# Kernel optimization log

Measured on AMD Instinct MI355X. Metric: run time of the kernel, lower is better.

Reference implementation:

```python
import jax, jax.numpy as jnp
import numpy as np

MARGIN = 0.2
EPS = 1e-6  # torch.pairwise_distance adds eps to the difference before the norm


def setup_inputs() -> dict:
    key = jax.random.key(0)
    k1, k2, k3 = jax.random.split(key, 3)
    B, D = 8192, 128
    emb1 = jax.random.normal(k1, (B, D), dtype=jnp.float32)
    emb2 = jax.random.normal(k2, (B, D), dtype=jnp.float32)
    target = jax.random.randint(k3, (B,), 0, 2, dtype=jnp.int64)
    return {"emb1": emb1, "emb2": emb2, "target": target}


def reference(emb1, emb2, target):
    B, D = emb1.shape
    # torch.pairwise_distance(a, b) = ||a - b + EPS||_2; expand the square:
    # |a-b+eps|^2 = |a|^2 + |b|^2 - 2 a.b + 2*eps*(sum(a)-sum(b)) + D*eps^2
    sq = (
        jnp.sum(emb1 * emb1, axis=-1)[:, None]
        + jnp.sum(emb2 * emb2, axis=-1)[None, :]
        - 2.0 * (emb1 @ emb2.T)
        + 2.0 * EPS * (jnp.sum(emb1, axis=-1)[:, None] - jnp.sum(emb2, axis=-1)[None, :])
        + D * EPS * EPS
    )
    dist = jnp.sqrt(jnp.maximum(sq, 0.0))  # [B, B]: dist[i, j] = ||emb1[i] - emb2[j] + eps||

    pos = target == 1
    neg = target == 0
    # hardest positive: max over columns j with target[j]==1; hardest negative: min over target[j]==0
    pos_max = jnp.max(jnp.where(pos[None, :], dist, -jnp.inf), axis=1)  # [B]
    neg_min = jnp.min(jnp.where(neg[None, :], dist, jnp.inf), axis=1)   # [B]
    per_anchor = jnp.maximum(pos_max - neg_min + MARGIN, 0.0)
    anchor_w = pos.astype(dist.dtype)
    # mean over anchors (rows i with target[i]==1)
    return jnp.sum(per_anchor * anchor_w) / jnp.sum(anchor_w)
```

## Files before the change

kernel.cpp:

```cpp
#include <hip/hip_runtime.h>
#include <hip/hip_bf16.h>
#include <math.h>


#define DDIM   128
#define SPLITS 8
#define MARGIN 0.2f
#define EPS    1e-6f
#define SENT   1e30f

#define CHUNK_PITCH 1056
#define WAVE_SPAN   (8 * CHUNK_PITCH)
#define TILE_BYTES  (4 * WAVE_SPAN)

typedef unsigned short ushort_t;
typedef __attribute__((ext_vector_type(8))) short short8;
typedef __attribute__((ext_vector_type(4))) float f32x4;

__device__ __forceinline__ ushort_t f2bf(float f) {
    unsigned int u = __float_as_uint(f);
    u = (u + 0x7FFFu + ((u >> 16) & 1u)) >> 16;
    return (ushort_t)u;
}

__device__ __forceinline__ void g2lds16(const ushort_t* g, void* lds) {
    __builtin_amdgcn_global_load_lds(
        (const __attribute__((address_space(1))) unsigned int*)g,
        (__attribute__((address_space(3))) unsigned int*)lds,
        16, 0, 0);
}

__global__ void prep_kernel(const float* __restrict__ e1, const float* __restrict__ e2,
                            const int* __restrict__ target,
                            ushort_t* __restrict__ e1b, ushort_t* __restrict__ e2b,
                            float* __restrict__ rowterm,
                            float* __restrict__ cpos, float* __restrict__ cneg,
                            float* __restrict__ redsum, int* __restrict__ ticket, int B) {
    if (blockIdx.x == 0 && threadIdx.x == 0) {
        redsum[0] = 0.f; redsum[1] = 0.f; *ticket = 0;
    }
    int w    = (blockIdx.x * blockDim.x + threadIdx.x) >> 6;
    int lane = threadIdx.x & 63;
    if (w >= 2 * B) return;
    bool first = (w < B);
    int r = first ? w : w - B;
    const float* src = (first ? e1 : e2) + (size_t)r * DDIM;
    float2 v = *(const float2*)(src + lane * 2);
    ushort_t* dst = (first ? e1b : e2b) + (size_t)r * DDIM;
    ushort2 o;
    if (first) { o.x = f2bf(-2.f * v.x); o.y = f2bf(-2.f * v.y); }
    else       { o.x = f2bf(v.x);        o.y = f2bf(v.y); }
    *(ushort2*)(dst + lane * 2) = o;
    float s = v.x + v.y;
    float n = v.x * v.x + v.y * v.y;
    #pragma unroll
    for (int off = 32; off > 0; off >>= 1) {
        s += __shfl_down(s, off, 64);
        n += __shfl_down(n, off, 64);
    }
    if (lane == 0) {
        if (first) {
            rowterm[r] = n + 2.f * EPS * s + (float)DDIM * EPS * EPS;
        } else {
            float ct = n - 2.f * EPS * s;
            int tg = target[r];
            cpos[r] = (tg == 1) ? ct : -SENT;
            cneg[r] = (tg == 0) ? ct :  SENT;
        }
    }
}

__device__ __forceinline__ void stage_tile_dma(const ushort_t* __restrict__ gRow0,
                                               unsigned char* __restrict__ lds,
                                               int w, int l) {
    const ushort_t* g = gRow0 + (size_t)(w * 32) * DDIM + l * 8;
    unsigned char* lp = lds + w * WAVE_SPAN;
    #pragma unroll
    for (int it = 0; it < 8; ++it)
        g2lds16(g + it * 512, lp + it * CHUNK_PITCH);
}

__global__ __launch_bounds__(256, 2)
void tile_kernel(const ushort_t* __restrict__ e1b, const ushort_t* __restrict__ e2b,
                 const float* __restrict__ cpos, const float* __restrict__ cneg,
                 float* __restrict__ pmp, float* __restrict__ nmp, int B) {
    __shared__ __align__(16) unsigned char Bs[2][TILE_BYTES];

    const int tid = threadIdx.x;
    const int w   = tid >> 6;
    const int l   = tid & 63;
    const int lq  = l >> 4;
    const int lm  = l & 15;
    const int row0 = blockIdx.x * 128;
    const int colSpan = B / SPLITS;
    const int col0 = blockIdx.y * colSpan;
    const int nTiles = colSpan / 128;

    const int wr = (w >> 1) * 64;
    const int wc = (w & 1) * 64;

    const unsigned char* bLane0 = Bs[0] + ((wc >> 2) + (lm >> 2)) * CHUNK_PITCH
                                        + (lm & 3) * 256 + lq * 16;

    const ushort_t* aG = e1b + (size_t)(row0 + wr + lm) * DDIM + lq * 8;
    short8 afr[4][4];
    #pragma unroll
    for (int i = 0; i < 4; ++i)
        #pragma unroll
        for (int k4 = 0; k4 < 4; ++k4)
            afr[i][k4] = *(const short8*)(aG + i * 16 * DDIM + k4 * 32);

    stage_tile_dma(e2b + (size_t)col0 * DDIM, Bs[0], w, l);

    float pm[4][4], nm[4][4];
    #pragma unroll
    for (int i = 0; i < 4; ++i)
        #pragma unroll
        for (int r = 0; r < 4; ++r) { pm[i][r] = -SENT; nm[i][r] = SENT; }

    __syncthreads();

    for (int t = 0; t < nTiles; ++t) {
        if (t + 1 < nTiles)
            stage_tile_dma(e2b + (size_t)(col0 + (t + 1) * 128) * DDIM,
                           Bs[(t + 1) & 1], w, l);

        const unsigned char* bl = bLane0 + (t & 1) * TILE_BYTES;

        f32x4 acc[4][4];
        #pragma unroll
        for (int i = 0; i < 4; ++i)
            #pragma unroll
            for (int j = 0; j < 4; ++j)
                acc[i][j] = (f32x4){0.f, 0.f, 0.f, 0.f};

        #pragma unroll
        for (int kk = 0; kk < DDIM; kk += 32) {
            const int k4 = kk >> 5;
            const int ko = kk * 2;
            short8 bf[4];
            #pragma unroll
            for (int j = 0; j < 4; ++j)
                bf[j] = *(const short8*)(bl + j * (4 * CHUNK_PITCH) + ko);
            #pragma unroll
            for (int i = 0; i < 4; ++i)
                #pragma unroll
                for (int j = 0; j < 4; ++j)
                    acc[i][j] = __builtin_amdgcn_mfma_f32_16x16x32_bf16(
                                    afr[i][k4], bf[j], acc[i][j], 0, 0, 0);
        }

        {
            const int colb = col0 + t * 128 + wc + lm;
            #pragma unroll
            for (int jp = 0; jp < 2; ++jp) {
                const int j0 = 2 * jp, j1 = j0 + 1;
                const float cp0 = cpos[colb + j0 * 16], cn0 = cneg[colb + j0 * 16];
                const float cp1 = cpos[colb + j1 * 16], cn1 = cneg[colb + j1 * 16];
                #pragma unroll
                for (int i = 0; i < 4; ++i)
                    #pragma unroll
                    for (int r = 0; r < 4; ++r) {
                        const float d0 = acc[i][j0][r];
                        const float d1 = acc[i][j1][r];
                        pm[i][r] = fmaxf(fmaxf(pm[i][r], d0 + cp0), d1 + cp1);
                        nm[i][r] = fminf(fminf(nm[i][r], d0 + cn0), d1 + cn1);
                    }
            }
        }

        __syncthreads();
    }

    #pragma unroll
    for (int m = 1; m < 16; m <<= 1) {
        #pragma unroll
        for (int i = 0; i < 4; ++i)
            #pragma unroll
            for (int r = 0; r < 4; ++r) {
                pm[i][r] = fmaxf(pm[i][r], __shfl_xor(pm[i][r], m, 64));
                nm[i][r] = fminf(nm[i][r], __shfl_xor(nm[i][r], m, 64));
            }
    }

    float* smP = (float*)Bs;
    float* smN = smP + 128;
    if ((w & 1) == 1 && lm == 0) {
        #pragma unroll
        for (int i = 0; i < 4; ++i)
            #pragma unroll
            for (int r = 0; r < 4; ++r) {
                int lr = wr + i * 16 + lq * 4 + r;
                smP[lr] = pm[i][r];
                smN[lr] = nm[i][r];
            }
    }
    __syncthreads();
    if ((w & 1) == 0 && lm == 0) {
        #pragma unroll
        for (int i = 0; i < 4; ++i)
            #pragma unroll
            for (int r = 0; r < 4; ++r) {
                int lr  = wr + i * 16 + lq * 4 + r;
                int row = row0 + lr;
                pmp[(size_t)blockIdx.y * B + row] = fmaxf(pm[i][r], smP[lr]);
                nmp[(size_t)blockIdx.y * B + row] = fminf(nm[i][r], smN[lr]);
            }
    }
}

__global__ void reduce_kernel(const float* __restrict__ pmp, const float* __restrict__ nmp,
                              const float* __restrict__ rowterm, const int* __restrict__ target,
                              float* __restrict__ redsum, int* __restrict__ ticket,
                              float* __restrict__ out, int B) {
    int row = blockIdx.x * blockDim.x + threadIdx.x;
    float s = 0.f, c = 0.f;
    {
        float pmv = -SENT, nmv = SENT;
        #pragma unroll
        for (int sp = 0; sp < SPLITS; ++sp) {
            pmv = fmaxf(pmv, pmp[(size_t)sp * B + row]);
            nmv = fminf(nmv, nmp[(size_t)sp * B + row]);
        }
        float rt = rowterm[row];
        float dp = sqrtf(fmaxf(rt + pmv, 0.f));
        float dn = sqrtf(fmaxf(rt + nmv, 0.f));
        if (target[row] == 1) {
            s = fmaxf(dp - dn + MARGIN, 0.f);
            c = 1.f;
        }
    }
    #pragma unroll
    for (int off = 32; off > 0; off >>= 1) {
        s += __shfl_down(s, off, 64);
        c += __shfl_down(c, off, 64);
    }
    __shared__ float ls[4], lc[4];
    int wv = threadIdx.x >> 6, ln = threadIdx.x & 63;
    if (ln == 0) { ls[wv] = s; lc[wv] = c; }
    __syncthreads();
    if (threadIdx.x == 0) {
        float ss = ls[0] + ls[1] + ls[2] + ls[3];
        float cc = lc[0] + lc[1] + lc[2] + lc[3];
        atomicAdd(&redsum[0], ss);
        atomicAdd(&redsum[1], cc);
        __threadfence();
        int done = atomicAdd(ticket, 1);
        if (done == (int)gridDim.x - 1) {
            __threadfence();
            float fs = __hip_atomic_load(&redsum[0], __ATOMIC_RELAXED, __HIP_MEMORY_SCOPE_AGENT);
            float fc = __hip_atomic_load(&redsum[1], __ATOMIC_RELAXED, __HIP_MEMORY_SCOPE_AGENT);
            out[0] = fs / fc;
        }
    }
}

extern "C" void kernel_launch(void* const* d_in, const int* in_sizes, int n_in,
                              void* d_out, int out_size, void* d_ws, size_t ws_size,
                              hipStream_t stream) {
    const float* e1     = (const float*)d_in[0];
    const float* e2     = (const float*)d_in[1];
    const int*   target = (const int*)d_in[2];
    float* out = (float*)d_out;
    const int B = in_sizes[2];

    char* p = (char*)d_ws;
    ushort_t* e1b  = (ushort_t*)p;   p += (size_t)B * DDIM * 2;
    ushort_t* e2b  = (ushort_t*)p;   p += (size_t)B * DDIM * 2;
    float* rowterm = (float*)p;      p += (size_t)B * 4;
    float* cpos    = (float*)p;      p += (size_t)B * 4;
    float* cneg    = (float*)p;      p += (size_t)B * 4;
    float* pmp     = (float*)p;      p += (size_t)SPLITS * B * 4;
    float* nmp     = (float*)p;      p += (size_t)SPLITS * B * 4;
    float* redsum  = (float*)p;      p += 2 * 4;
    int*   ticket  = (int*)p;

    {
        int blocks = (2 * B + 3) / 4;
        prep_kernel<<<blocks, 256, 0, stream>>>(e1, e2, target, e1b, e2b,
                                                rowterm, cpos, cneg, redsum, ticket, B);
    }
    {
        dim3 grid(B / 128, SPLITS);
        tile_kernel<<<grid, 256, 0, stream>>>(e1b, e2b, cpos, cneg, pmp, nmp, B);
    }
    reduce_kernel<<<32, 256, 0, stream>>>(pmp, nmp, rowterm, target,
                                          redsum, ticket, out, B);
}
```

Measured before the change: 92.67 us.

## Fuse final reduction into tile kernel via per-row-block tickets; vectorize prep

Removes the separate reduce kernel launch. Each tile block increments a per-row-block ticket, and the last of the SPLITS blocks for that row block combines the partial max/min values, computes the per-anchor hinge terms and atomically accumulates them into the global sum. A global ticket then lets the final block write the mean. The prep kernel is also reworked to use 8 lanes per row with float4 loads and xor shuffles instead of a full wave per row. The aim is to cut launch overhead and improve prep memory efficiency, at the cost of extra atomics and fences in the tile kernel.

```diff
diff --git a/kernel.cpp b/kernel.cpp
--- a/kernel.cpp
+++ b/kernel.cpp
@@ -16,6 +16,7 @@
 typedef unsigned short ushort_t;
 typedef __attribute__((ext_vector_type(8))) short short8;
 typedef __attribute__((ext_vector_type(4))) float f32x4;
+typedef __attribute__((ext_vector_type(4))) unsigned short ushort4_t;
 
 __device__ __forceinline__ ushort_t f2bf(float f) {
     unsigned int u = __float_as_uint(f);
@@ -35,30 +36,39 @@
                             ushort_t* __restrict__ e1b, ushort_t* __restrict__ e2b,
                             float* __restrict__ rowterm,
                             float* __restrict__ cpos, float* __restrict__ cneg,
-                            float* __restrict__ redsum, int* __restrict__ ticket, int B) {
-    if (blockIdx.x == 0 && threadIdx.x == 0) {
-        redsum[0] = 0.f; redsum[1] = 0.f; *ticket = 0;
-    }
-    int w    = (blockIdx.x * blockDim.x + threadIdx.x) >> 6;
-    int lane = threadIdx.x & 63;
-    if (w >= 2 * B) return;
-    bool first = (w < B);
-    int r = first ? w : w - B;
+                            float* __restrict__ redsum, int* __restrict__ ticket,
+                            int* __restrict__ rbTicket, int B) {
+    if (blockIdx.x == 0) {
+        int t = threadIdx.x;
+        if (t < B / 128) rbTicket[t] = 0;
+        else if (t == 64) { redsum[0] = 0.f; redsum[1] = 0.f; }
+        else if (t == 65) *ticket = 0;
+    }
+    int gr  = blockIdx.x * 32 + (threadIdx.x >> 3);
+    int seg = threadIdx.x & 7;
+    bool first = gr < B;
+    int r = first ? gr : gr - B;
     const float* src = (first ? e1 : e2) + (size_t)r * DDIM;
-    float2 v = *(const float2*)(src + lane * 2);
-    ushort_t* dst = (first ? e1b : e2b) + (size_t)r * DDIM;
-    ushort2 o;
-    if (first) { o.x = f2bf(-2.f * v.x); o.y = f2bf(-2.f * v.y); }
-    else       { o.x = f2bf(v.x);        o.y = f2bf(v.y); }
-    *(ushort2*)(dst + lane * 2) = o;
-    float s = v.x + v.y;
-    float n = v.x * v.x + v.y * v.y;
-    #pragma unroll
-    for (int off = 32; off > 0; off >>= 1) {
-        s += __shfl_down(s, off, 64);
-        n += __shfl_down(n, off, 64);
-    }
-    if (lane == 0) {
+    ushort_t*    dst = (first ? e1b : e2b) + (size_t)r * DDIM;
+    const float sc = first ? -2.f : 1.f;
+    float s = 0.f, n = 0.f;
+    #pragma unroll
+    for (int it = 0; it < 4; ++it) {
+        int e0 = (seg + it * 8) * 4;
+        float4 v = *(const float4*)(src + e0);
+        ushort4_t o;
+        o.x = f2bf(sc * v.x); o.y = f2bf(sc * v.y);
+        o.z = f2bf(sc * v.z); o.w = f2bf(sc * v.w);
+        *(ushort4_t*)(dst + e0) = o;
+        s += v.x + v.y + v.z + v.w;
+        n += v.x * v.x + v.y * v.y + v.z * v.z + v.w * v.w;
+    }
+    #pragma unroll
+    for (int m = 1; m <= 4; m <<= 1) {
+        s += __shfl_xor(s, m, 64);
+        n += __shfl_xor(n, m, 64);
+    }
+    if (seg == 0) {
         if (first) {
             rowterm[r] = n + 2.f * EPS * s + (float)DDIM * EPS * EPS;
         } else {
@@ -83,7 +93,10 @@
 __global__ __launch_bounds__(256, 2)
 void tile_kernel(const ushort_t* __restrict__ e1b, const ushort_t* __restrict__ e2b,
                  const float* __restrict__ cpos, const float* __restrict__ cneg,
-                 float* __restrict__ pmp, float* __restrict__ nmp, int B) {
+                 const float* __restrict__ rowterm, const int* __restrict__ target,
+                 float* __restrict__ pmp, float* __restrict__ nmp,
+                 int* __restrict__ rbTicket, float* __restrict__ redsum,
+                 int* __restrict__ ticket, float* __restrict__ out, int B) {
     __shared__ __align__(16) unsigned char Bs[2][TILE_BYTES];
 
     const int tid = threadIdx.x;
@@ -207,20 +220,28 @@
                 nmp[(size_t)blockIdx.y * B + row] = fminf(nm[i][r], smN[lr]);
             }
     }
-}
-
-__global__ void reduce_kernel(const float* __restrict__ pmp, const float* __restrict__ nmp,
-                              const float* __restrict__ rowterm, const int* __restrict__ target,
-                              float* __restrict__ redsum, int* __restrict__ ticket,
-                              float* __restrict__ out, int B) {
-    int row = blockIdx.x * blockDim.x + threadIdx.x;
+
+    __shared__ int lastrb;
+    __syncthreads();
+    if (tid == 0) {
+        __threadfence();
+        int prev = __hip_atomic_fetch_add(&rbTicket[blockIdx.x], 1,
+                       __ATOMIC_ACQ_REL, __HIP_MEMORY_SCOPE_AGENT);
+        lastrb = (prev == SPLITS - 1);
+    }
+    __syncthreads();
+    if (!lastrb) return;
+
     float s = 0.f, c = 0.f;
-    {
+    if (tid < 128) {
+        int row = row0 + tid;
         float pmv = -SENT, nmv = SENT;
         #pragma unroll
         for (int sp = 0; sp < SPLITS; ++sp) {
-            pmv = fmaxf(pmv, pmp[(size_t)sp * B + row]);
-            nmv = fminf(nmv, nmp[(size_t)sp * B + row]);
+            pmv = fmaxf(pmv, __hip_atomic_load(&pmp[(size_t)sp * B + row],
+                              __ATOMIC_RELAXED, __HIP_MEMORY_SCOPE_AGENT));
+            nmv = fminf(nmv, __hip_atomic_load(&nmp[(size_t)sp * B + row],
+                              __ATOMIC_RELAXED, __HIP_MEMORY_SCOPE_AGENT));
         }
         float rt = rowterm[row];
         float dp = sqrtf(fmaxf(rt + pmv, 0.f));
@@ -236,17 +257,16 @@
         c += __shfl_down(c, off, 64);
     }
     __shared__ float ls[4], lc[4];
-    int wv = threadIdx.x >> 6, ln = threadIdx.x & 63;
-    if (ln == 0) { ls[wv] = s; lc[wv] = c; }
-    __syncthreads();
-    if (threadIdx.x == 0) {
+    if (l == 0) { ls[w] = s; lc[w] = c; }
+    __syncthreads();
+    if (tid == 0) {
         float ss = ls[0] + ls[1] + ls[2] + ls[3];
         float cc = lc[0] + lc[1] + lc[2] + lc[3];
         atomicAdd(&redsum[0], ss);
         atomicAdd(&redsum[1], cc);
         __threadfence();
         int done = atomicAdd(ticket, 1);
-        if (done == (int)gridDim.x - 1) {
+        if (done == (B / 128) - 1) {
             __threadfence();
             float fs = __hip_atomic_load(&redsum[0], __ATOMIC_RELAXED, __HIP_MEMORY_SCOPE_AGENT);
             float fc = __hip_atomic_load(&redsum[1], __ATOMIC_RELAXED, __HIP_MEMORY_SCOPE_AGENT);
@@ -273,17 +293,19 @@
     float* pmp     = (float*)p;      p += (size_t)SPLITS * B * 4;
     float* nmp     = (float*)p;      p += (size_t)SPLITS * B * 4;
     float* redsum  = (float*)p;      p += 2 * 4;
-    int*   ticket  = (int*)p;
+    int*   ticket  = (int*)p;        p += 4;
+    int*   rbTicket= (int*)p;        p += (size_t)(B / 128) * 4;
 
     {
-        int blocks = (2 * B + 3) / 4;
+        int blocks = (2 * B) / 32;
         prep_kernel<<<blocks, 256, 0, stream>>>(e1, e2, target, e1b, e2b,
-                                                rowterm, cpos, cneg, redsum, ticket, B);
+                                                rowterm, cpos, cneg,
+                                                redsum, ticket, rbTicket, B);
     }
     {
         dim3 grid(B / 128, SPLITS);
-        tile_kernel<<<grid, 256, 0, stream>>>(e1b, e2b, cpos, cneg, pmp, nmp, B);
-    }
-    reduce_kernel<<<32, 256, 0, stream>>>(pmp, nmp, rowterm, target,
-                                          redsum, ticket, out, B);
-}
+        tile_kernel<<<grid, 256, 0, stream>>>(e1b, e2b, cpos, cneg,
+                                              rowterm, target, pmp, nmp,
+                                              rbTicket, redsum, ticket, out, B);
+    }
+}
```

New measurement: 104.2 us. +12.4%, slower.
